# Performance work log

Measured on AMD Instinct MI355X. Metric: run time of the kernel, lower is better.

Reference implementation:

```python
import jax, jax.numpy as jnp
import numpy as np


def _squash(x, eps=1e-8):
    # squash along last (feature) dim: v = s * ||s||^2 / (1+||s||^2) / ||s||
    n2 = jnp.sum(x * x, axis=-1, keepdims=True)
    return x * (n2 / (1.0 + n2)) / jnp.sqrt(n2 + eps)


def setup_inputs() -> dict:
    key = jax.random.key(0)
    k1, k2 = jax.random.split(key)
    B, N_IN, N_CAPS, N_FEAT = 16, 2048, 64, 16
    inputs = jax.random.normal(k1, (B, N_IN, N_CAPS, N_FEAT), dtype=jnp.float32)
    bias = jax.random.normal(k2, (N_CAPS, N_FEAT), dtype=jnp.float32) * 0.02
    return {"inputs": inputs, "bias": bias, "num_routing": 3}


def reference(inputs, bias, num_routing):
    # inputs: [B, n_in, n_caps, n_feat]; bias: [n_caps, n_feat]
    priors = jnp.zeros_like(inputs)
    outputs = None
    for i in range(num_routing):
        agreements = jax.nn.softmax(priors, axis=-2)            # over n_caps
        outputs = jnp.sum(inputs * agreements, axis=-3, keepdims=True)  # [B,1,n_caps,n_feat]
        outputs = _squash(outputs + bias)
        if i < num_routing - 1:
            priors = priors + jnp.sum(inputs * outputs, axis=-1, keepdims=True)
    return outputs[:, 0]  # [B, n_caps, n_feat]
```

## Files before the change

kernel.cpp:

```cpp
#include <hip/hip_runtime.h>
#include <math.h>

#define BB 16
#define NIN 2048
#define NC 64
#define NF 16
#define BLOCKS_PER_B 128
#define I_PER_BLOCK (NIN / BLOCKS_PER_B)
#define I_PER_WAVE (I_PER_BLOCK / 4)
#define NPART (BB * BLOCKS_PER_B)

__device__ __forceinline__ float dot4(float4 a, float4 b) {
    return a.x * b.x + a.y * b.y + a.z * b.z + a.w * b.w;
}

__global__ __launch_bounds__(256) void pass_mean(const float* __restrict__ in,
                                                 float* __restrict__ part) {
    const int b = blockIdx.x >> 7;
    const int blk = blockIdx.x & 127;
    const int lane = threadIdx.x & 63;
    const int wave = threadIdx.x >> 6;
    const float4* in4 = (const float4*)in;

    float4 acc[4];
#pragma unroll
    for (int k = 0; k < 4; ++k) acc[k] = make_float4(0.f, 0.f, 0.f, 0.f);

    const size_t base =
        ((size_t)b * NIN + (size_t)blk * I_PER_BLOCK + (size_t)wave * I_PER_WAVE) * 256;
#pragma unroll
    for (int t = 0; t < I_PER_WAVE; ++t) {
        const float4* p = in4 + base + (size_t)t * 256;
#pragma unroll
        for (int k = 0; k < 4; ++k) {
            float4 v = p[lane + (k << 6)];
            acc[k].x += v.x; acc[k].y += v.y; acc[k].z += v.z; acc[k].w += v.w;
        }
    }

    __shared__ float4 red[4 * 256];
#pragma unroll
    for (int k = 0; k < 4; ++k) red[wave * 256 + lane + (k << 6)] = acc[k];
    __syncthreads();

    const int t = threadIdx.x;
    float4 s0 = red[t], s1 = red[256 + t], s2 = red[512 + t], s3 = red[768 + t];
    float4* g = (float4*)(part + (size_t)blockIdx.x * 1024) + t;
    *g = make_float4(s0.x + s1.x + s2.x + s3.x, s0.y + s1.y + s2.y + s3.y,
                     s0.z + s1.z + s2.z + s3.z, s0.w + s1.w + s2.w + s3.w);
}

__global__ __launch_bounds__(256) void pass_route(const float* __restrict__ in,
                                                  const float* __restrict__ wv,
                                                  float* __restrict__ part) {
    const int b = blockIdx.x >> 7;
    const int blk = blockIdx.x & 127;
    const int lane = threadIdx.x & 63;
    const int wave = threadIdx.x >> 6;
    const float4* in4 = (const float4*)in;
    const float4* wv4 = (const float4*)wv + (size_t)b * 256;

    float4 ow[4];
#pragma unroll
    for (int k = 0; k < 4; ++k) ow[k] = wv4[lane + (k << 6)];

    float4 acc[4];
#pragma unroll
    for (int k = 0; k < 4; ++k) acc[k] = make_float4(0.f, 0.f, 0.f, 0.f);

    const size_t base =
        ((size_t)b * NIN + (size_t)blk * I_PER_BLOCK + (size_t)wave * I_PER_WAVE) * 256;
    for (int t = 0; t < I_PER_WAVE; ++t) {
        const float4* p = in4 + base + (size_t)t * 256;
        float4 v[4];
        float d[4];
#pragma unroll
        for (int k = 0; k < 4; ++k) v[k] = p[lane + (k << 6)];
#pragma unroll
        for (int k = 0; k < 4; ++k) {
            d[k] = dot4(v[k], ow[k]);
            d[k] += __shfl_xor(d[k], 1);
            d[k] += __shfl_xor(d[k], 2);
        }
        float m = fmaxf(fmaxf(d[0], d[1]), fmaxf(d[2], d[3]));
        m = fmaxf(m, __shfl_xor(m, 4));
        m = fmaxf(m, __shfl_xor(m, 8));
        m = fmaxf(m, __shfl_xor(m, 16));
        m = fmaxf(m, __shfl_xor(m, 32));
        float e[4];
        float ssum = 0.f;
#pragma unroll
        for (int k = 0; k < 4; ++k) {
            e[k] = __expf(d[k] - m);
            ssum += e[k];
        }
        ssum += __shfl_xor(ssum, 4);
        ssum += __shfl_xor(ssum, 8);
        ssum += __shfl_xor(ssum, 16);
        ssum += __shfl_xor(ssum, 32);
        const float inv = 1.0f / ssum;
#pragma unroll
        for (int k = 0; k < 4; ++k) {
            const float a = e[k] * inv;
            acc[k].x += a * v[k].x;
            acc[k].y += a * v[k].y;
            acc[k].z += a * v[k].z;
            acc[k].w += a * v[k].w;
        }
    }

    __shared__ float4 red[4 * 256];
#pragma unroll
    for (int k = 0; k < 4; ++k) red[wave * 256 + lane + (k << 6)] = acc[k];
    __syncthreads();

    const int t = threadIdx.x;
    float4 s0 = red[t], s1 = red[256 + t], s2 = red[512 + t], s3 = red[768 + t];
    float4* g = (float4*)(part + (size_t)blockIdx.x * 1024) + t;
    *g = make_float4(s0.x + s1.x + s2.x + s3.x, s0.y + s1.y + s2.y + s3.y,
                     s0.z + s1.z + s2.z + s3.z, s0.w + s1.w + s2.w + s3.w);
}

__global__ __launch_bounds__(256) void reduce_squash(const float* __restrict__ part,
                                                     const float* __restrict__ bias,
                                                     const float* __restrict__ prev,
                                                     float* __restrict__ dst,
                                                     float scale) {
    const int b = blockIdx.x >> 6;
    const int c = blockIdx.x & 63;
    const int tid = threadIdx.x;
    const int f = tid & 15;
    const int pc = tid >> 4;

    const float* p = part + (size_t)(b * BLOCKS_PER_B) * 1024 + c * NF + f;
    float sum = 0.f;
#pragma unroll
    for (int j = 0; j < 8; ++j) sum += p[(size_t)(pc + 16 * j) * 1024];

    __shared__ float red[256];
    red[tid] = sum;
    __syncthreads();
    if (tid < 128) red[tid] += red[tid + 128];
    __syncthreads();
    if (tid < 64) red[tid] += red[tid + 64];
    __syncthreads();
    if (tid < 32) red[tid] += red[tid + 32];
    __syncthreads();
    if (tid < 16) {
        float s = (red[tid] + red[tid + 16]) * scale + bias[c * NF + f];
        float n2 = s * s;
        n2 += __shfl_xor(n2, 1);
        n2 += __shfl_xor(n2, 2);
        n2 += __shfl_xor(n2, 4);
        n2 += __shfl_xor(n2, 8);
        const float sc = n2 / (1.0f + n2) / sqrtf(n2 + 1e-8f);
        float o = s * sc;
        const size_t oi = (size_t)b * 1024 + c * NF + f;
        if (prev) o += prev[oi];
        dst[oi] = o;
    }
}

extern "C" void kernel_launch(void* const* d_in, const int* in_sizes, int n_in,
                              void* d_out, int out_size, void* d_ws, size_t ws_size,
                              hipStream_t stream) {
    const float* in = (const float*)d_in[0];
    const float* bias = (const float*)d_in[1];

    float* ws = (float*)d_ws;
    float* part = ws;
    float* out0 = ws + (size_t)NPART * 1024;
    float* osum = out0 + 16384;

    dim3 grid(BB * BLOCKS_PER_B), blk(256);
    pass_mean<<<grid, blk, 0, stream>>>(in, part);
    reduce_squash<<<1024, 256, 0, stream>>>(part, bias, nullptr, out0, 1.0f / 64.0f);
    pass_route<<<grid, blk, 0, stream>>>(in, out0, part);
    reduce_squash<<<1024, 256, 0, stream>>>(part, bias, out0, osum, 1.0f);
    pass_route<<<grid, blk, 0, stream>>>(in, osum, part);
    reduce_squash<<<1024, 256, 0, stream>>>(part, bias, nullptr, (float*)d_out, 1.0f);
}
```

Measured before the change: 89.92 us.

## Cache an fp16 copy of inputs for the routing passes

The first mean pass now also writes a half-precision copy of the inputs into workspace. Both routing passes read that copy and convert it back to fp32 in registers. This halves the bytes read in the two later passes at the cost of one extra write pass. It also adds fp16 rounding error to the routing logits and weighted sums.

```diff
diff --git a/kernel.cpp b/kernel.cpp
--- a/kernel.cpp
+++ b/kernel.cpp
@@ -1,4 +1,5 @@
 #include <hip/hip_runtime.h>
+#include <hip/hip_fp16.h>
 #include <math.h>
 
 #define BB 16
@@ -14,8 +15,17 @@
     return a.x * b.x + a.y * b.y + a.z * b.z + a.w * b.w;
 }
 
+__device__ __forceinline__ float4 half4_to_float4(uint2 u) {
+    __half2 h0 = *reinterpret_cast<__half2*>(&u.x);
+    __half2 h1 = *reinterpret_cast<__half2*>(&u.y);
+    float2 f0 = __half22float2(h0);
+    float2 f1 = __half22float2(h1);
+    return make_float4(f0.x, f0.y, f1.x, f1.y);
+}
+
 __global__ __launch_bounds__(256) void pass_mean(const float* __restrict__ in,
-                                                 float* __restrict__ part) {
+                                                 float* __restrict__ part,
+                                                 uint2* __restrict__ cp) {
     const int b = blockIdx.x >> 7;
     const int blk = blockIdx.x & 127;
     const int lane = threadIdx.x & 63;
@@ -31,10 +41,17 @@
 #pragma unroll
     for (int t = 0; t < I_PER_WAVE; ++t) {
         const float4* p = in4 + base + (size_t)t * 256;
+        uint2* q = cp + base + (size_t)t * 256;
 #pragma unroll
         for (int k = 0; k < 4; ++k) {
             float4 v = p[lane + (k << 6)];
             acc[k].x += v.x; acc[k].y += v.y; acc[k].z += v.z; acc[k].w += v.w;
+            __half2 h0 = __float22half2_rn(make_float2(v.x, v.y));
+            __half2 h1 = __float22half2_rn(make_float2(v.z, v.w));
+            uint2 u;
+            u.x = *reinterpret_cast<unsigned*>(&h0);
+            u.y = *reinterpret_cast<unsigned*>(&h1);
+            q[lane + (k << 6)] = u;
         }
     }
 
@@ -50,14 +67,13 @@
                      s0.z + s1.z + s2.z + s3.z, s0.w + s1.w + s2.w + s3.w);
 }
 
-__global__ __launch_bounds__(256) void pass_route(const float* __restrict__ in,
+__global__ __launch_bounds__(256) void pass_route(const uint2* __restrict__ in2,
                                                   const float* __restrict__ wv,
                                                   float* __restrict__ part) {
     const int b = blockIdx.x >> 7;
     const int blk = blockIdx.x & 127;
     const int lane = threadIdx.x & 63;
     const int wave = threadIdx.x >> 6;
-    const float4* in4 = (const float4*)in;
     const float4* wv4 = (const float4*)wv + (size_t)b * 256;
 
     float4 ow[4];
@@ -71,11 +87,11 @@
     const size_t base =
         ((size_t)b * NIN + (size_t)blk * I_PER_BLOCK + (size_t)wave * I_PER_WAVE) * 256;
     for (int t = 0; t < I_PER_WAVE; ++t) {
-        const float4* p = in4 + base + (size_t)t * 256;
+        const uint2* p = in2 + base + (size_t)t * 256;
         float4 v[4];
         float d[4];
 #pragma unroll
-        for (int k = 0; k < 4; ++k) v[k] = p[lane + (k << 6)];
+        for (int k = 0; k < 4; ++k) v[k] = half4_to_float4(p[lane + (k << 6)]);
 #pragma unroll
         for (int k = 0; k < 4; ++k) {
             d[k] = dot4(v[k], ow[k]);
@@ -171,12 +187,13 @@
     float* part = ws;
     float* out0 = ws + (size_t)NPART * 1024;
     float* osum = out0 + 16384;
+    uint2* cp = (uint2*)(osum + 16384);
 
     dim3 grid(BB * BLOCKS_PER_B), blk(256);
-    pass_mean<<<grid, blk, 0, stream>>>(in, part);
+    pass_mean<<<grid, blk, 0, stream>>>(in, part, cp);
     reduce_squash<<<1024, 256, 0, stream>>>(part, bias, nullptr, out0, 1.0f / 64.0f);
-    pass_route<<<grid, blk, 0, stream>>>(in, out0, part);
+    pass_route<<<grid, blk, 0, stream>>>(cp, out0, part);
     reduce_squash<<<1024, 256, 0, stream>>>(part, bias, out0, osum, 1.0f);
-    pass_route<<<grid, blk, 0, stream>>>(in, osum, part);
+    pass_route<<<grid, blk, 0, stream>>>(cp, osum, part);
     reduce_squash<<<1024, 256, 0, stream>>>(part, bias, nullptr, (float*)d_out, 1.0f);
 }
```

New measurement: 80.98 us. 1.11x faster.

## Cache fp16 copy of inputs in first pass and stream it in routing passes

Applied to the files above, without the earlier changes.

The mean pass now writes a half-precision copy of the 128 MB input to workspace, and both routing passes read that 64 MB copy instead of the fp32 input. Partial sums are also stored in fp16, and the block count per batch is halved with a new lane-to-feature mapping. This cuts HBM traffic in the routing passes at the cost of an extra 64 MB write in the first pass and reduced precision in the agreements and partials, which may affect accuracy tolerance.

```diff
diff --git a/kernel.cpp b/kernel.cpp
--- a/kernel.cpp
+++ b/kernel.cpp
@@ -1,127 +1,166 @@
 #include <hip/hip_runtime.h>
+#include <hip/hip_fp16.h>
 #include <math.h>
 
 #define BB 16
 #define NIN 2048
 #define NC 64
 #define NF 16
-#define BLOCKS_PER_B 128
-#define I_PER_BLOCK (NIN / BLOCKS_PER_B)
-#define I_PER_WAVE (I_PER_BLOCK / 4)
-#define NPART (BB * BLOCKS_PER_B)
+#define BLOCKS_PER_B 64
+#define NPBLK (BB * BLOCKS_PER_B)
 
 __device__ __forceinline__ float dot4(float4 a, float4 b) {
     return a.x * b.x + a.y * b.y + a.z * b.z + a.w * b.w;
 }
 
+__device__ __forceinline__ unsigned pack2(float x, float y) {
+    __half2 h = __float22half2_rn(make_float2(x, y));
+    return *reinterpret_cast<unsigned*>(&h);
+}
+
+__device__ __forceinline__ float2 unpack2(unsigned u) {
+    __half2 h = *reinterpret_cast<__half2*>(&u);
+    return __half22float2(h);
+}
+
+__device__ __forceinline__ float4 unpack4(unsigned a, unsigned b) {
+    float2 f0 = unpack2(a), f1 = unpack2(b);
+    return make_float4(f0.x, f0.y, f1.x, f1.y);
+}
+
 __global__ __launch_bounds__(256) void pass_mean(const float* __restrict__ in,
-                                                 float* __restrict__ part) {
-    const int b = blockIdx.x >> 7;
-    const int blk = blockIdx.x & 127;
+                                                 uint2* __restrict__ part2,
+                                                 uint4* __restrict__ cp) {
+    const int b = blockIdx.x >> 6;
+    const int blk = blockIdx.x & 63;
     const int lane = threadIdx.x & 63;
     const int wave = threadIdx.x >> 6;
+
     const float4* in4 = (const float4*)in;
 
     float4 acc[4];
 #pragma unroll
     for (int k = 0; k < 4; ++k) acc[k] = make_float4(0.f, 0.f, 0.f, 0.f);
 
-    const size_t base =
-        ((size_t)b * NIN + (size_t)blk * I_PER_BLOCK + (size_t)wave * I_PER_WAVE) * 256;
-#pragma unroll
-    for (int t = 0; t < I_PER_WAVE; ++t) {
-        const float4* p = in4 + base + (size_t)t * 256;
-#pragma unroll
-        for (int k = 0; k < 4; ++k) {
-            float4 v = p[lane + (k << 6)];
-            acc[k].x += v.x; acc[k].y += v.y; acc[k].z += v.z; acc[k].w += v.w;
+#pragma unroll
+    for (int t = 0; t < 8; ++t) {
+        const size_t i = (size_t)b * NIN + blk * 32 + wave * 8 + t;
+        const size_t row = i * 256;
+#pragma unroll
+        for (int k = 0; k < 2; ++k) {
+            float4 v0 = in4[row + 2 * (lane + 64 * k)];
+            float4 v1 = in4[row + 2 * (lane + 64 * k) + 1];
+            acc[2 * k].x += v0.x; acc[2 * k].y += v0.y;
+            acc[2 * k].z += v0.z; acc[2 * k].w += v0.w;
+            acc[2 * k + 1].x += v1.x; acc[2 * k + 1].y += v1.y;
+            acc[2 * k + 1].z += v1.z; acc[2 * k + 1].w += v1.w;
+            uint4 u;
+            u.x = pack2(v0.x, v0.y); u.y = pack2(v0.z, v0.w);
+            u.z = pack2(v1.x, v1.y); u.w = pack2(v1.z, v1.w);
+            cp[i * 128 + lane + 64 * k] = u;
         }
     }
 
     __shared__ float4 red[4 * 256];
-#pragma unroll
-    for (int k = 0; k < 4; ++k) red[wave * 256 + lane + (k << 6)] = acc[k];
+    const int s0a = 2 * lane, s0b = 2 * lane + 128;
+    red[wave * 256 + s0a] = acc[0];
+    red[wave * 256 + s0a + 1] = acc[1];
+    red[wave * 256 + s0b] = acc[2];
+    red[wave * 256 + s0b + 1] = acc[3];
     __syncthreads();
 
     const int t = threadIdx.x;
-    float4 s0 = red[t], s1 = red[256 + t], s2 = red[512 + t], s3 = red[768 + t];
-    float4* g = (float4*)(part + (size_t)blockIdx.x * 1024) + t;
-    *g = make_float4(s0.x + s1.x + s2.x + s3.x, s0.y + s1.y + s2.y + s3.y,
-                     s0.z + s1.z + s2.z + s3.z, s0.w + s1.w + s2.w + s3.w);
-}
-
-__global__ __launch_bounds__(256) void pass_route(const float* __restrict__ in,
+    float4 s = red[t];
+#pragma unroll
+    for (int w = 1; w < 4; ++w) {
+        float4 r = red[w * 256 + t];
+        s.x += r.x; s.y += r.y; s.z += r.z; s.w += r.w;
+    }
+    uint2 o;
+    o.x = pack2(s.x, s.y);
+    o.y = pack2(s.z, s.w);
+    part2[blockIdx.x * 256 + t] = o;
+}
+
+__global__ __launch_bounds__(256) void pass_route(const uint4* __restrict__ cp,
                                                   const float* __restrict__ wv,
-                                                  float* __restrict__ part) {
-    const int b = blockIdx.x >> 7;
-    const int blk = blockIdx.x & 127;
+                                                  uint2* __restrict__ part2) {
+    const int b = blockIdx.x >> 6;
+    const int blk = blockIdx.x & 63;
     const int lane = threadIdx.x & 63;
     const int wave = threadIdx.x >> 6;
-    const float4* in4 = (const float4*)in;
     const float4* wv4 = (const float4*)wv + (size_t)b * 256;
 
     float4 ow[4];
-#pragma unroll
-    for (int k = 0; k < 4; ++k) ow[k] = wv4[lane + (k << 6)];
+    ow[0] = wv4[2 * lane];
+    ow[1] = wv4[2 * lane + 1];
+    ow[2] = wv4[2 * lane + 128];
+    ow[3] = wv4[2 * lane + 129];
 
     float4 acc[4];
 #pragma unroll
     for (int k = 0; k < 4; ++k) acc[k] = make_float4(0.f, 0.f, 0.f, 0.f);
 
-    const size_t base =
-        ((size_t)b * NIN + (size_t)blk * I_PER_BLOCK + (size_t)wave * I_PER_WAVE) * 256;
-    for (int t = 0; t < I_PER_WAVE; ++t) {
-        const float4* p = in4 + base + (size_t)t * 256;
-        float4 v[4];
-        float d[4];
-#pragma unroll
-        for (int k = 0; k < 4; ++k) v[k] = p[lane + (k << 6)];
-#pragma unroll
-        for (int k = 0; k < 4; ++k) {
-            d[k] = dot4(v[k], ow[k]);
-            d[k] += __shfl_xor(d[k], 1);
-            d[k] += __shfl_xor(d[k], 2);
-        }
-        float m = fmaxf(fmaxf(d[0], d[1]), fmaxf(d[2], d[3]));
+#pragma unroll
+    for (int t = 0; t < 8; ++t) {
+        const size_t i = (size_t)b * NIN + blk * 32 + wave * 8 + t;
+        const uint4 u0 = cp[i * 128 + lane];
+        const uint4 u1 = cp[i * 128 + lane + 64];
+        float4 v00 = unpack4(u0.x, u0.y), v01 = unpack4(u0.z, u0.w);
+        float4 v10 = unpack4(u1.x, u1.y), v11 = unpack4(u1.z, u1.w);
+
+        float d0 = dot4(v00, ow[0]) + dot4(v01, ow[1]);
+        float d1 = dot4(v10, ow[2]) + dot4(v11, ow[3]);
+        d0 += __shfl_xor(d0, 1);
+        d1 += __shfl_xor(d1, 1);
+
+        float m = fmaxf(d0, d1);
+        m = fmaxf(m, __shfl_xor(m, 2));
         m = fmaxf(m, __shfl_xor(m, 4));
         m = fmaxf(m, __shfl_xor(m, 8));
         m = fmaxf(m, __shfl_xor(m, 16));
         m = fmaxf(m, __shfl_xor(m, 32));
-        float e[4];
-        float ssum = 0.f;
-#pragma unroll
-        for (int k = 0; k < 4; ++k) {
-            e[k] = __expf(d[k] - m);
-            ssum += e[k];
-        }
-        ssum += __shfl_xor(ssum, 4);
-        ssum += __shfl_xor(ssum, 8);
-        ssum += __shfl_xor(ssum, 16);
-        ssum += __shfl_xor(ssum, 32);
-        const float inv = 1.0f / ssum;
-#pragma unroll
-        for (int k = 0; k < 4; ++k) {
-            const float a = e[k] * inv;
-            acc[k].x += a * v[k].x;
-            acc[k].y += a * v[k].y;
-            acc[k].z += a * v[k].z;
-            acc[k].w += a * v[k].w;
-        }
+        float e0 = __expf(d0 - m), e1 = __expf(d1 - m);
+        float ss = e0 + e1;
+        ss += __shfl_xor(ss, 2);
+        ss += __shfl_xor(ss, 4);
+        ss += __shfl_xor(ss, 8);
+        ss += __shfl_xor(ss, 16);
+        ss += __shfl_xor(ss, 32);
+        const float inv = 1.0f / ss;
+        const float a0 = e0 * inv, a1 = e1 * inv;
+        acc[0].x += a0 * v00.x; acc[0].y += a0 * v00.y;
+        acc[0].z += a0 * v00.z; acc[0].w += a0 * v00.w;
+        acc[1].x += a0 * v01.x; acc[1].y += a0 * v01.y;
+        acc[1].z += a0 * v01.z; acc[1].w += a0 * v01.w;
+        acc[2].x += a1 * v10.x; acc[2].y += a1 * v10.y;
+        acc[2].z += a1 * v10.z; acc[2].w += a1 * v10.w;
+        acc[3].x += a1 * v11.x; acc[3].y += a1 * v11.y;
+        acc[3].z += a1 * v11.z; acc[3].w += a1 * v11.w;
     }
 
     __shared__ float4 red[4 * 256];
-#pragma unroll
-    for (int k = 0; k < 4; ++k) red[wave * 256 + lane + (k << 6)] = acc[k];
+    const int s0a = 2 * lane, s0b = 2 * lane + 128;
+    red[wave * 256 + s0a] = acc[0];
+    red[wave * 256 + s0a + 1] = acc[1];
+    red[wave * 256 + s0b] = acc[2];
+    red[wave * 256 + s0b + 1] = acc[3];
     __syncthreads();
 
     const int t = threadIdx.x;
-    float4 s0 = red[t], s1 = red[256 + t], s2 = red[512 + t], s3 = red[768 + t];
-    float4* g = (float4*)(part + (size_t)blockIdx.x * 1024) + t;
-    *g = make_float4(s0.x + s1.x + s2.x + s3.x, s0.y + s1.y + s2.y + s3.y,
-                     s0.z + s1.z + s2.z + s3.z, s0.w + s1.w + s2.w + s3.w);
-}
-
-__global__ __launch_bounds__(256) void reduce_squash(const float* __restrict__ part,
+    float4 s = red[t];
+#pragma unroll
+    for (int w = 1; w < 4; ++w) {
+        float4 r = red[w * 256 + t];
+        s.x += r.x; s.y += r.y; s.z += r.z; s.w += r.w;
+    }
+    uint2 o;
+    o.x = pack2(s.x, s.y);
+    o.y = pack2(s.z, s.w);
+    part2[blockIdx.x * 256 + t] = o;
+}
+
+__global__ __launch_bounds__(256) void reduce_squash(const uint2* __restrict__ part2,
                                                      const float* __restrict__ bias,
                                                      const float* __restrict__ prev,
                                                      float* __restrict__ dst,
@@ -129,16 +168,28 @@
     const int b = blockIdx.x >> 6;
     const int c = blockIdx.x & 63;
     const int tid = threadIdx.x;
-    const int f = tid & 15;
-    const int pc = tid >> 4;
-
-    const float* p = part + (size_t)(b * BLOCKS_PER_B) * 1024 + c * NF + f;
-    float sum = 0.f;
-#pragma unroll
-    for (int j = 0; j < 8; ++j) sum += p[(size_t)(pc + 16 * j) * 1024];
+    const int q = tid >> 2;
+    const int h4 = tid & 3;
+
+    const uint2 u = part2[(size_t)(b * BLOCKS_PER_B + q) * 256 + c * 4 + h4];
+    const float4 f = unpack4(u.x, u.y);
+
+    __shared__ float lds[1024];
+    lds[q * 16 + h4 * 4 + 0] = f.x;
+    lds[q * 16 + h4 * 4 + 1] = f.y;
+    lds[q * 16 + h4 * 4 + 2] = f.z;
+    lds[q * 16 + h4 * 4 + 3] = f.w;
+    __syncthreads();
 
     __shared__ float red[256];
-    red[tid] = sum;
+    {
+        const int f16 = tid & 15;
+        const int qg = tid >> 4;
+        float s = 0.f;
+#pragma unroll
+        for (int j = 0; j < 4; ++j) s += lds[(qg * 4 + j) * 16 + f16];
+        red[tid] = s;
+    }
     __syncthreads();
     if (tid < 128) red[tid] += red[tid + 128];
     __syncthreads();
@@ -147,7 +198,7 @@
     if (tid < 32) red[tid] += red[tid + 32];
     __syncthreads();
     if (tid < 16) {
-        float s = (red[tid] + red[tid + 16]) * scale + bias[c * NF + f];
+        float s = (red[tid] + red[tid + 16]) * scale + bias[c * NF + tid];
         float n2 = s * s;
         n2 += __shfl_xor(n2, 1);
         n2 += __shfl_xor(n2, 2);
@@ -155,7 +206,7 @@
         n2 += __shfl_xor(n2, 8);
         const float sc = n2 / (1.0f + n2) / sqrtf(n2 + 1e-8f);
         float o = s * sc;
-        const size_t oi = (size_t)b * 1024 + c * NF + f;
+        const size_t oi = (size_t)b * 1024 + c * NF + tid;
         if (prev) o += prev[oi];
         dst[oi] = o;
     }
@@ -168,15 +219,16 @@
     const float* bias = (const float*)d_in[1];
 
     float* ws = (float*)d_ws;
-    float* part = ws;
-    float* out0 = ws + (size_t)NPART * 1024;
+    uint2* part2 = (uint2*)ws;
+    float* out0 = ws + (size_t)NPBLK * 512;
     float* osum = out0 + 16384;
-
-    dim3 grid(BB * BLOCKS_PER_B), blk(256);
-    pass_mean<<<grid, blk, 0, stream>>>(in, part);
-    reduce_squash<<<1024, 256, 0, stream>>>(part, bias, nullptr, out0, 1.0f / 64.0f);
-    pass_route<<<grid, blk, 0, stream>>>(in, out0, part);
-    reduce_squash<<<1024, 256, 0, stream>>>(part, bias, out0, osum, 1.0f);
-    pass_route<<<grid, blk, 0, stream>>>(in, osum, part);
-    reduce_squash<<<1024, 256, 0, stream>>>(part, bias, nullptr, (float*)d_out, 1.0f);
-}
+    uint4* cp = (uint4*)(osum + 16384);
+
+    dim3 grid(NPBLK), blk(256);
+    pass_mean<<<grid, blk, 0, stream>>>(in, part2, cp);
+    reduce_squash<<<1024, 256, 0, stream>>>(part2, bias, nullptr, out0, 1.0f / 64.0f);
+    pass_route<<<grid, blk, 0, stream>>>(cp, out0, part2);
+    reduce_squash<<<1024, 256, 0, stream>>>(part2, bias, out0, osum, 1.0f);
+    pass_route<<<grid, blk, 0, stream>>>(cp, osum, part2);
+    reduce_squash<<<1024, 256, 0, stream>>>(part2, bias, nullptr, (float*)d_out, 1.0f);
+}
```

Result: faster. 85.90 us (-4.5%).
